# Performance work log

Measured on AMD Instinct MI355X. Metric: run time of the kernel, lower is better.

## Reference

```python
import jax, jax.numpy as jnp
import numpy as np
from jax import lax

MODEL_DIM = 384
KERNEL = 15
PAD = (KERNEL - 1) // 2
BATCH = 4096


def fake_quant(x, bits):
    """Per-tensor symmetric fake quantization with straight-through estimator.
    scale = max|x| / qmax, q = clip(round(x/scale), qmin, qmax), dq = q*scale.
    """
    qmax = float(2 ** (bits - 1) - 1)
    qmin = -float(2 ** (bits - 1))
    scale = jnp.maximum(jnp.max(jnp.abs(x)) / qmax, jnp.asarray(1e-8, x.dtype))
    dq = jnp.clip(jnp.round(x / scale), qmin, qmax) * scale
    return x + lax.stop_gradient(dq - x)  # STE: identity gradient


def setup_inputs() -> dict:
    key = jax.random.key(0)
    k = jax.random.split(key, 7)
    image = jax.random.normal(k[0], (BATCH, 28, 28), dtype=jnp.float32)
    # LinearQuant(28 -> model_dim)
    W1 = jax.random.normal(k[1], (MODEL_DIM, 28), dtype=jnp.float32) * (1.0 / np.sqrt(28))
    b1 = jax.random.normal(k[2], (MODEL_DIM,), dtype=jnp.float32) * 0.01
    # depthwise Conv1DQuant(model_dim, model_dim, K, groups=model_dim): weight [C_out, 1, K]
    Wc = jax.random.normal(k[3], (MODEL_DIM, 1, KERNEL), dtype=jnp.float32) * (1.0 / np.sqrt(KERNEL))
    bc = jax.random.normal(k[4], (MODEL_DIM,), dtype=jnp.float32) * 0.01
    # LinearQuant(28*model_dim -> 10)
    Wf = jax.random.normal(k[5], (10, 28 * MODEL_DIM), dtype=jnp.float32) * (1.0 / np.sqrt(28 * MODEL_DIM))
    bf = jax.random.normal(k[6], (10,), dtype=jnp.float32) * 0.01
    return {"image": image, "W1": W1, "b1": b1, "Wc": Wc, "bc": bc, "Wf": Wf, "bf": bf}


def reference(image, W1, b1, Wc, bc, Wf, bf):
    inp = image.reshape(-1, 28, 28)
    # linear_1 with 8-bit activation fake-quant in and 3-bit weight fake-quant
    x = fake_quant(inp, 8)
    lin = jnp.einsum('blf,of->blo', x, fake_quant(W1, 3)) + b1  # [B,28,model_dim]
    out1 = jnp.tanh(fake_quant(lin, 8))
    # depthwise conv1d over length 28, channels model_dim
    xc = jnp.transpose(fake_quant(out1, 8), (0, 2, 1))  # [B,C,L]
    conv = lax.conv_general_dilated(
        xc, fake_quant(Wc, 3), window_strides=(1,), padding=[(PAD, PAD)],
        dimension_numbers=('NCH', 'OIH', 'NCH'), feature_group_count=MODEL_DIM)
    conv = conv + bc[None, :, None]                      # [B,C,L]
    conv = jnp.transpose(conv, (0, 2, 1))                # [B,L,C]
    out2 = jnp.tanh(fake_quant(conv, 8)).reshape(-1, MODEL_DIM * 28)
    # final linear
    logits = fake_quant(out2, 8) @ fake_quant(Wf, 3).T + bf  # [B,10]
    return fake_quant(logits, 8)
```

## Files before the change

kernel.cpp:

```cpp
#include <hip/hip_runtime.h>

#define BATCH 4096
#define MD 384
#define KW 15
#define PADW 7
#define LSEQ 28
#define FIN 28

#define NX (BATCH*LSEQ*FIN)


#define B_SCF  0
#define B_LUT1 256
#define B_LUT2 512
#define B_PT0  1024
#define B_PT1  33792
#define B_PT2  41984
#define B_PTL  50176
#define B_W1B  54272
#define B_WCQ  78848
#define B_WFB  84992
#define B_LG   192512
#define B_XQB  356352

typedef __bf16 bf16x8 __attribute__((ext_vector_type(8)));
typedef float f32x4 __attribute__((ext_vector_type(4)));
typedef int i32x4 __attribute__((ext_vector_type(4)));

#if __has_builtin(__builtin_amdgcn_sdot4)
#define SDOT4(a,b,c) __builtin_amdgcn_sdot4((a),(b),(c),false)
#else
__device__ __forceinline__ int SDOT4(int a,int b,int c){
  c += ((a<<24)>>24)*((b<<24)>>24);
  c += ((a<<16)>>24)*((b<<16)>>24);
  c += ((a<<8)>>24)*((b<<8)>>24);
  c += (a>>24)*(b>>24);
  return c;
}
#endif

#if __has_builtin(__builtin_amdgcn_alignbyte)
#define ALIGNB(hi,lo,s) __builtin_amdgcn_alignbyte((hi),(lo),(s))
#else
#define ALIGNB(hi,lo,s) ((int)(((unsigned)(lo)>>(8*(s)))|((unsigned)(hi)<<(32-8*(s)))))
#endif

__device__ __forceinline__ unsigned short f2bf(float f){
  return (unsigned short)(__float_as_uint(f)>>16);
}

__device__ __forceinline__ void blkStore4(float m0,float m1,float m2,float m3,float4* dst){
  #pragma unroll
  for(int off=32;off;off>>=1){
    m0=fmaxf(m0,__shfl_xor(m0,off,64));
    m1=fmaxf(m1,__shfl_xor(m1,off,64));
    m2=fmaxf(m2,__shfl_xor(m2,off,64));
    m3=fmaxf(m3,__shfl_xor(m3,off,64));
  }
  __shared__ float sm[4][4];
  int wid=threadIdx.x>>6;
  if((threadIdx.x&63)==0){sm[wid][0]=m0;sm[wid][1]=m1;sm[wid][2]=m2;sm[wid][3]=m3;}
  __syncthreads();
  if(threadIdx.x==0){
    for(int i=1;i<4;i++){
      m0=fmaxf(m0,sm[i][0]);m1=fmaxf(m1,sm[i][1]);
      m2=fmaxf(m2,sm[i][2]);m3=fmaxf(m3,sm[i][3]);
    }
    *dst=make_float4(m0,m1,m2,m3);
  }
}

__device__ __forceinline__ void blkStoreMM(float mn,float mx,float2* dst){
  #pragma unroll
  for(int off=32;off;off>>=1){
    mn=fminf(mn,__shfl_xor(mn,off,64));
    mx=fmaxf(mx,__shfl_xor(mx,off,64));
  }
  __shared__ float smn[8],smx[8];
  int wid=threadIdx.x>>6, nw=blockDim.x>>6;
  if((threadIdx.x&63)==0){smn[wid]=mn;smx[wid]=mx;}
  __syncthreads();
  if(threadIdx.x==0){
    for(int i=1;i<nw;i++){mn=fminf(mn,smn[i]);mx=fmaxf(mx,smx[i]);}
    *dst=make_float2(mn,mx);
  }
}

__global__ __launch_bounds__(256)
void k_maxabs_in(const float* __restrict__ img,const float* __restrict__ W1,
                 const float* __restrict__ Wc,const float* __restrict__ Wf,
                 float4* __restrict__ pt0){
  float m0=0.f,m1=0.f,m2=0.f,m3=0.f;
  const int N4=NX/4;
  const int NW1=MD*FIN, NWC=MD*KW, NWF=10*MD*LSEQ;
  const int total=N4+NW1+NWC+NWF;
  const float4* img4=(const float4*)img;
  for(int i=blockIdx.x*blockDim.x+threadIdx.x;i<total;i+=gridDim.x*blockDim.x){
    if(i<N4){
      float4 v=img4[i];
      m0=fmaxf(m0,fmaxf(fmaxf(fabsf(v.x),fabsf(v.y)),fmaxf(fabsf(v.z),fabsf(v.w))));
    }
    else if(i<N4+NW1) m1=fmaxf(m1,fabsf(W1[i-N4]));
    else if(i<N4+NW1+NWC) m2=fmaxf(m2,fabsf(Wc[i-N4-NW1]));
    else m3=fmaxf(m3,fabsf(Wf[i-N4-NW1-NWC]));
  }
  blkStore4(m0,m1,m2,m3,&pt0[blockIdx.x]);
}

__global__ __launch_bounds__(256)
void k_red0(const float4* __restrict__ pt,float* __restrict__ scf){
  int t=threadIdx.x;
  float m0=0.f,m1=0.f,m2=0.f,m3=0.f;
  for(int i=t;i<2048;i+=256){
    float4 v=pt[i];
    m0=fmaxf(m0,v.x);m1=fmaxf(m1,v.y);m2=fmaxf(m2,v.z);m3=fmaxf(m3,v.w);
  }
  #pragma unroll
  for(int off=32;off;off>>=1){
    m0=fmaxf(m0,__shfl_xor(m0,off,64));
    m1=fmaxf(m1,__shfl_xor(m1,off,64));
    m2=fmaxf(m2,__shfl_xor(m2,off,64));
    m3=fmaxf(m3,__shfl_xor(m3,off,64));
  }
  __shared__ float sm[4][4];
  int wid=t>>6;
  if((t&63)==0){sm[wid][0]=m0;sm[wid][1]=m1;sm[wid][2]=m2;sm[wid][3]=m3;}
  __syncthreads();
  if(t==0){
    for(int i=1;i<4;i++){
      m0=fmaxf(m0,sm[i][0]);m1=fmaxf(m1,sm[i][1]);
      m2=fmaxf(m2,sm[i][2]);m3=fmaxf(m3,sm[i][3]);
    }
    scf[0]=fmaxf(m0/127.f,1e-8f);
    scf[1]=fmaxf(m1/3.f,1e-8f);
    scf[2]=fmaxf(m2/3.f,1e-8f);
    scf[3]=fmaxf(m3/3.f,1e-8f);
  }
}

__global__ __launch_bounds__(256)
void k_redmm(const float2* __restrict__ pt,int n,float* __restrict__ scf,
             int preIdx,int outIdx,char* __restrict__ lutg){
  int t=threadIdx.x;
  float mn=1e30f,mx=-1e30f;
  for(int i=t;i<n;i+=256){
    float2 v=pt[i];
    mn=fminf(mn,v.x); mx=fmaxf(mx,v.y);
  }
  #pragma unroll
  for(int off=32;off;off>>=1){
    mn=fminf(mn,__shfl_xor(mn,off,64));
    mx=fmaxf(mx,__shfl_xor(mx,off,64));
  }
  __shared__ float smn[4],smx[4];
  __shared__ float bs,bso;
  int wid=t>>6;
  if((t&63)==0){smn[wid]=mn;smx[wid]=mx;}
  __syncthreads();
  if(t==0){
    for(int i=1;i<4;i++){mn=fminf(mn,smn[i]);mx=fmaxf(mx,smx[i]);}
    float ma=fmaxf(fabsf(mn),fabsf(mx));
    float s=fmaxf(ma/127.f,1e-8f);
    float a1=fabsf(fminf(fmaxf(rintf(mn/s),-128.f),127.f)*s);
    float a2=fabsf(fminf(fmaxf(rintf(mx/s),-128.f),127.f)*s);
    float so=fmaxf(tanhf(fmaxf(a1,a2))/127.f,1e-8f);
    scf[preIdx]=s; scf[outIdx]=so;
    bs=s; bso=so;
  }
  __syncthreads();
  float d=(float)(t-128)*bs;
  lutg[t]=(char)(int)fminf(fmaxf(rintf(tanhf(d)/bso),-128.f),127.f);
}

__global__ __launch_bounds__(256)
void k_prep(const float* __restrict__ img,const float* __restrict__ W1,
            const float* __restrict__ Wc,const float* __restrict__ Wf,
            const float* __restrict__ scf,char* __restrict__ wsb){
  float s_img=scf[0], s_w1=scf[1], s_wc=scf[2], s_wf=scf[3];
  float inv_img=1.f/s_img;
  unsigned short* xqb=(unsigned short*)(wsb+B_XQB);
  unsigned short* w1b=(unsigned short*)(wsb+B_W1B);
  char* wcpk=wsb+B_WCQ;
  char* wfb=wsb+B_WFB;
  const int T0=BATCH*LSEQ*32;
  const int T1=T0+MD*32;
  const int T2=T1+MD*16;
  const int T3=T2+10*10752;
  for(int i=blockIdx.x*blockDim.x+threadIdx.x;i<T3;i+=gridDim.x*blockDim.x){
    if(i<T0){
      int row=i>>5, cc=i&31;
      float q = cc<FIN ? fminf(fmaxf(rintf(img[row*FIN+cc]*inv_img),-128.f),127.f) : 0.f;
      xqb[i]=f2bf(q);
    } else if(i<T1){
      int j=i-T0; int o=j>>5, cc=j&31;
      float q = cc<FIN ? fminf(fmaxf(rintf(W1[o*FIN+cc]/s_w1),-4.f),3.f) : 0.f;
      w1b[j]=f2bf(q);
    } else if(i<T2){
      int j=i-T1; int c=j>>4, k=j&15;
      char q=0;
      if(k<KW) q=(char)(int)fminf(fmaxf(rintf(Wc[c*KW+k]/s_wc),-4.f),3.f);
      wcpk[j]=q;
    } else {
      int j=i-T2;
      int n=j/10752, r=j-n*10752;
      int c=r/28, l=r-c*28;
      wfb[j]=(char)(int)fminf(fmaxf(rintf(Wf[n*10752+l*MD+c]/s_wf),-4.f),3.f);
    }
  }
}

template<int MODE>
__global__ __launch_bounds__(512)
void k_fused(const unsigned short* __restrict__ xqb,const unsigned short* __restrict__ w1b,
             const float* __restrict__ b1,const float* __restrict__ scf,
             const char* __restrict__ lut1g,const char* __restrict__ lut2g,
             const char* __restrict__ wcpk,const float* __restrict__ bc,
             const int* __restrict__ wfw,const float* __restrict__ bfv,
             float2* __restrict__ ptmm,float* __restrict__ lg,
             float* __restrict__ ptl){
  __shared__ int ldsI[10752];
  __shared__ int psum[10][4][7];
  __shared__ char lutA[256];
  __shared__ char lutB[256];
  int t=threadIdx.x, wid=t>>6, lane=t&63, l4=lane>>4, l15=lane&15;
  {
    const int* src=(const int*)w1b;
    for(int i=t;i<6144;i+=512) ldsI[i]=src[i];
  }
  __syncthreads();
  unsigned short* Wlds=(unsigned short*)ldsI;
  bf16x8 bfr[3]; float b1v[3];
  #pragma unroll
  for(int ni=0;ni<3;ni++){
    int o=(wid*3+ni)*16+l15;
    bfr[ni]=*(const bf16x8*)&Wlds[o*32+l4*8];
    b1v[ni]=b1[o];
  }
  bf16x8 af[7];
  int r0=blockIdx.x*112;
  #pragma unroll
  for(int mt=0;mt<7;mt++)
    af[mt]=*(const bf16x8*)&xqb[(size_t)(r0+mt*16+l15)*32+l4*8];
  float sg=scf[0]*scf[1];
  float inv_lin=1.f, inv_cv=1.f, sfac=1.f, gsc=1.f;
  if constexpr(MODE>=1){
    inv_lin=1.f/scf[4];
    sfac=scf[5]*scf[2];
    if(t<64) ((int*)lutA)[t]=((const int*)lut1g)[t];
  }
  if constexpr(MODE==2){
    inv_cv=1.f/scf[6];
    gsc=scf[3]*scf[7];
    if(t>=64&&t<128) ((int*)lutB)[t-64]=((const int*)lut2g)[t-64];
  }
  if constexpr(MODE>=1) __syncthreads();

  float mn=1e30f,mx=-1e30f;
  f32x4 zero={0.f,0.f,0.f,0.f};
  #pragma unroll
  for(int ni=0;ni<3;ni++){
    int o=(wid*3+ni)*16+l15;
    #pragma unroll
    for(int mt=0;mt<7;mt++){
      f32x4 acc=__builtin_amdgcn_mfma_f32_16x16x32_bf16(af[mt],bfr[ni],zero,0,0,0);
      if constexpr(MODE==0){
        #pragma unroll
        for(int r=0;r<4;r++){
          float v=sg*acc[r]+b1v[ni];
          mn=fminf(mn,v); mx=fmaxf(mx,v);
        }
      } else {
        unsigned w=0;
        #pragma unroll
        for(int r=0;r<4;r++){
          float v=sg*acc[r]+b1v[ni];
          int ql=(int)fminf(fmaxf(rintf(v*inv_lin),-128.f),127.f);
          unsigned q=(unsigned)(unsigned char)lutA[ql+128];
          w|=q<<(8*r);
        }
        ldsI[o*28+mt*4+l4]=(int)w;
      }
    }
  }
  if constexpr(MODE==0){
    blkStoreMM(mn,mx,&ptmm[blockIdx.x]);
    return;
  }
  __syncthreads();

  int oww[3][7];
  float mnc=1e30f,mxc=-1e30f;
  #pragma unroll
  for(int rr=0;rr<3;rr++){
    int j=t+rr*512;
    int s=j/384, c=j-s*384;
    i32x4 wq=*(const i32x4*)(wcpk+(size_t)c*16);
    float bias=bc[c];
    int ext[11];
    ext[0]=0; ext[1]=0; ext[9]=0; ext[10]=0;
    #pragma unroll
    for(int i=0;i<7;i++) ext[2+i]=ldsI[c*28+s*7+i];
    #pragma unroll
    for(int l=0;l<LSEQ;l++){
      const int eb=l+1, bi=eb>>2, sh=eb&3;
      int A0,A1,A2,A3;
      if(sh==0){A0=ext[bi];A1=ext[bi+1];A2=ext[bi+2];A3=ext[bi+3];}
      else{
        A0=ALIGNB(ext[bi+1],ext[bi],sh);
        A1=ALIGNB(ext[bi+2],ext[bi+1],sh);
        A2=ALIGNB(ext[bi+3],ext[bi+2],sh);
        A3=ALIGNB(ext[bi+4],ext[bi+3],sh);
      }
      int idot=SDOT4(A0,wq[0],SDOT4(A1,wq[1],SDOT4(A2,wq[2],SDOT4(A3,wq[3],0))));
      float v=fmaf((float)idot,sfac,bias);
      if constexpr(MODE==1){
        mnc=fminf(mnc,v); mxc=fmaxf(mxc,v);
      } else {
        int qc=(int)fminf(fmaxf(rintf(v*inv_cv),-128.f),127.f);
        unsigned q2=(unsigned)(unsigned char)lutB[qc+128];
        if((l&3)==0) oww[rr][l>>2]=(int)q2;
        else oww[rr][l>>2]|=(int)(q2<<(8*(l&3)));
      }
    }
  }
  if constexpr(MODE==1){
    blkStoreMM(mnc,mxc,&ptmm[blockIdx.x]);
    return;
  }

  __syncthreads();
  #pragma unroll
  for(int rr=0;rr<3;rr++){
    int j=t+rr*512;
    int s=j/384, c=j-s*384;
    #pragma unroll
    for(int i=0;i<7;i++) ldsI[s*2688+c*7+i]=oww[rr][i];
  }
  __syncthreads();

  if(t<448){
    int cwv[24];
    #pragma unroll
    for(int s=0;s<4;s++)
      #pragma unroll
      for(int j6=0;j6<6;j6++) cwv[s*6+j6]=ldsI[s*2688+j6*448+t];
    #pragma unroll
    for(int o=0;o<10;o++){
      int a0=0,a1=0,a2=0,a3=0;
      #pragma unroll
      for(int j6=0;j6<6;j6++){
        int wfv=wfw[o*2688+j6*448+t];
        a0=SDOT4(cwv[0*6+j6],wfv,a0);
        a1=SDOT4(cwv[1*6+j6],wfv,a1);
        a2=SDOT4(cwv[2*6+j6],wfv,a2);
        a3=SDOT4(cwv[3*6+j6],wfv,a3);
      }
      #pragma unroll
      for(int off=32;off;off>>=1){
        a0+=__shfl_xor(a0,off,64);
        a1+=__shfl_xor(a1,off,64);
        a2+=__shfl_xor(a2,off,64);
        a3+=__shfl_xor(a3,off,64);
      }
      if(lane==0){
        psum[o][0][wid]=a0; psum[o][1][wid]=a1;
        psum[o][2][wid]=a2; psum[o][3][wid]=a3;
      }
    }
  }
  __syncthreads();
  float m=0.f;
  if(t<40){
    int s=t/10, o=t-s*10;
    int sum=0;
    #pragma unroll
    for(int i=0;i<7;i++) sum+=psum[o][s][i];
    float v=fmaf((float)sum,gsc,bfv[o]);
    lg[(blockIdx.x*4+s)*10+o]=v;
    m=fabsf(v);
  }
  if(t<64){
    #pragma unroll
    for(int off=32;off;off>>=1) m=fmaxf(m,__shfl_xor(m,off,64));
    if(t==0) ptl[blockIdx.x]=m;
  }
}

__global__ __launch_bounds__(256)
void k_final(const float* __restrict__ lg,const float* __restrict__ ptl,
             float* __restrict__ out){
  int t=threadIdx.x;
  float m=0.f;
  for(int i=t;i<1024;i+=256) m=fmaxf(m,ptl[i]);
  #pragma unroll
  for(int off=32;off;off>>=1) m=fmaxf(m,__shfl_xor(m,off,64));
  __shared__ float sm[4];
  __shared__ float sv;
  int wid=t>>6;
  if((t&63)==0) sm[wid]=m;
  __syncthreads();
  if(t==0){
    for(int k=1;k<4;k++) m=fmaxf(m,sm[k]);
    sv=fmaxf(m/127.f,1e-8f);
  }
  __syncthreads();
  float s=sv;
  int i=blockIdx.x*256+t;
  out[i]=fminf(fmaxf(rintf(lg[i]/s),-128.f),127.f)*s;
}

extern "C" void kernel_launch(void* const* d_in, const int* in_sizes, int n_in,
                              void* d_out, int out_size, void* d_ws, size_t ws_size,
                              hipStream_t stream){
  const float* img=(const float*)d_in[0];
  const float* W1 =(const float*)d_in[1];
  const float* b1 =(const float*)d_in[2];
  const float* Wc =(const float*)d_in[3];
  const float* bc =(const float*)d_in[4];
  const float* Wf =(const float*)d_in[5];
  const float* bf =(const float*)d_in[6];
  float* out=(float*)d_out;
  char* wsb=(char*)d_ws;
  float* scf=(float*)(wsb+B_SCF);
  float4* pt0=(float4*)(wsb+B_PT0);
  float2* pt1=(float2*)(wsb+B_PT1);
  float2* pt2=(float2*)(wsb+B_PT2);
  float* ptl=(float*)(wsb+B_PTL);
  float* lg=(float*)(wsb+B_LG);
  const unsigned short* xqb=(const unsigned short*)(wsb+B_XQB);
  const unsigned short* w1b=(const unsigned short*)(wsb+B_W1B);
  const char* wcpk=wsb+B_WCQ;
  const int* wfw=(const int*)(wsb+B_WFB);

  k_maxabs_in<<<2048,256,0,stream>>>(img,W1,Wc,Wf,pt0);
  k_red0<<<1,256,0,stream>>>(pt0,scf);
  k_prep<<<4096,256,0,stream>>>(img,W1,Wc,Wf,scf,wsb);
  k_fused<0><<<1024,512,0,stream>>>(xqb,w1b,b1,scf,nullptr,nullptr,wcpk,bc,wfw,bf,pt1,nullptr,nullptr);
  k_redmm<<<1,256,0,stream>>>(pt1,1024,scf,4,5,wsb+B_LUT1);
  k_fused<1><<<1024,512,0,stream>>>(xqb,w1b,b1,scf,wsb+B_LUT1,nullptr,wcpk,bc,wfw,bf,pt2,nullptr,nullptr);
  k_redmm<<<1,256,0,stream>>>(pt2,1024,scf,6,7,wsb+B_LUT2);
  k_fused<2><<<1024,512,0,stream>>>(xqb,w1b,b1,scf,wsb+B_LUT1,wsb+B_LUT2,wcpk,bc,wfw,bf,nullptr,lg,ptl);
  k_final<<<160,256,0,stream>>>(lg,ptl,out);
}
```

Before: 107.7 us.

## Use int8 MFMA for final linear, bpermute LUTs, hoisted min/max and padded LDS

The final 10-output linear layer now runs on int8 MFMA (16x16x64) over a byte-laid-out weight buffer instead of per-thread sdot4 with wave shuffle reductions. The LDS lookup tables are replaced by per-wave ds_bpermute lookups from a register-held 256-byte table. Scale and bias are folded into a single fma with a med3 clamp. The min/max passes now track raw accumulator extremes and apply the affine transform once at the end. LDS row strides are padded (29, 2692) to reduce bank conflicts, and the workspace offsets are moved to hold the larger weight buffer. This depends on k_prep writing Wf in the layout the new MFMA reads, which is not visible here.

Result: faster. 105.6 us (-2.0%).

```diff
diff --git a/kernel.cpp b/kernel.cpp
--- a/kernel.cpp
+++ b/kernel.cpp
@@ -20,8 +20,8 @@
 #define B_W1B  54272
 #define B_WCQ  78848
 #define B_WFB  84992
-#define B_LG   192512
-#define B_XQB  356352
+#define B_LG   257024
+#define B_XQB  420864
 
 typedef __bf16 bf16x8 __attribute__((ext_vector_type(8)));
 typedef float f32x4 __attribute__((ext_vector_type(4)));
@@ -47,6 +47,11 @@
 
 __device__ __forceinline__ unsigned short f2bf(float f){
   return (unsigned short)(__float_as_uint(f)>>16);
+}
+
+__device__ __forceinline__ unsigned lut_bperm(int iw,int lutw){
+  int res=__builtin_amdgcn_ds_bpermute(iw,lutw);
+  return ((unsigned)res>>(8*(iw&3)))&0xFFu;
 }
 
 __device__ __forceinline__ void blkStore4(float m0,float m1,float m2,float m3,float4* dst){
@@ -209,19 +214,19 @@
   }
 }
 
+#define CWS 29
+#define DWS 2692
 template<int MODE>
 __global__ __launch_bounds__(512)
 void k_fused(const unsigned short* __restrict__ xqb,const unsigned short* __restrict__ w1b,
              const float* __restrict__ b1,const float* __restrict__ scf,
              const char* __restrict__ lut1g,const char* __restrict__ lut2g,
              const char* __restrict__ wcpk,const float* __restrict__ bc,
-             const int* __restrict__ wfw,const float* __restrict__ bfv,
+             const char* __restrict__ wfb,const float* __restrict__ bfv,
              float2* __restrict__ ptmm,float* __restrict__ lg,
              float* __restrict__ ptl){
-  __shared__ int ldsI[10752];
-  __shared__ int psum[10][4][7];
-  __shared__ char lutA[256];
-  __shared__ char lutB[256];
+  __shared__ int ldsI[MD*CWS];
+  __shared__ int psumN[8][10][4];
   int t=threadIdx.x, wid=t>>6, lane=t&63, l4=lane>>4, l15=lane&15;
   {
     const int* src=(const int*)w1b;
@@ -242,21 +247,28 @@
   for(int mt=0;mt<7;mt++)
     af[mt]=*(const bf16x8*)&xqb[(size_t)(r0+mt*16+l15)*32+l4*8];
   float sg=scf[0]*scf[1];
-  float inv_lin=1.f, inv_cv=1.f, sfac=1.f, gsc=1.f;
+  float sgi=sg, b1s[3]={0.f,0.f,0.f};
+  int lutA_w=0,lutB_w=0;
+  float ck1=1.f,inv_cv=1.f,sfac=1.f,gsc=1.f;
   if constexpr(MODE>=1){
-    inv_lin=1.f/scf[4];
+    float inv_lin=1.f/scf[4];
+    sgi=sg*inv_lin;
+    #pragma unroll
+    for(int ni=0;ni<3;ni++) b1s[ni]=fmaf(b1v[ni],inv_lin,128.f);
+    lutA_w=((const int*)lut1g)[lane];
     sfac=scf[5]*scf[2];
-    if(t<64) ((int*)lutA)[t]=((const int*)lut1g)[t];
   }
   if constexpr(MODE==2){
     inv_cv=1.f/scf[6];
+    ck1=sfac*inv_cv;
     gsc=scf[3]*scf[7];
-    if(t>=64&&t<128) ((int*)lutB)[t-64]=((const int*)lut2g)[t-64];
+    lutB_w=((const int*)lut2g)[lane];
   }
   if constexpr(MODE>=1) __syncthreads();
 
+  f32x4 zero={0.f,0.f,0.f,0.f};
   float mn=1e30f,mx=-1e30f;
-  f32x4 zero={0.f,0.f,0.f,0.f};
+  float mnn[3]={1e30f,1e30f,1e30f},mxx[3]={-1e30f,-1e30f,-1e30f};
   #pragma unroll
   for(int ni=0;ni<3;ni++){
     int o=(wid*3+ni)*16+l15;
@@ -266,23 +278,26 @@
       if constexpr(MODE==0){
         #pragma unroll
         for(int r=0;r<4;r++){
-          float v=sg*acc[r]+b1v[ni];
-          mn=fminf(mn,v); mx=fmaxf(mx,v);
+          mnn[ni]=fminf(mnn[ni],acc[r]); mxx[ni]=fmaxf(mxx[ni],acc[r]);
         }
       } else {
         unsigned w=0;
         #pragma unroll
         for(int r=0;r<4;r++){
-          float v=sg*acc[r]+b1v[ni];
-          int ql=(int)fminf(fmaxf(rintf(v*inv_lin),-128.f),127.f);
-          unsigned q=(unsigned)(unsigned char)lutA[ql+128];
-          w|=q<<(8*r);
+          float x=fmaf(acc[r],sgi,b1s[ni]);
+          int iw=(int)__builtin_amdgcn_fmed3f(rintf(x),0.f,255.f);
+          w|=lut_bperm(iw,lutA_w)<<(8*r);
         }
-        ldsI[o*28+mt*4+l4]=(int)w;
+        ldsI[o*CWS+mt*4+l4]=(int)w;
       }
     }
   }
   if constexpr(MODE==0){
+    #pragma unroll
+    for(int ni=0;ni<3;ni++){
+      mn=fminf(mn,fmaf(mnn[ni],sg,b1v[ni]));
+      mx=fmaxf(mx,fmaf(mxx[ni],sg,b1v[ni]));
+    }
     blkStoreMM(mn,mx,&ptmm[blockIdx.x]);
     return;
   }
@@ -295,11 +310,14 @@
     int j=t+rr*512;
     int s=j/384, c=j-s*384;
     i32x4 wq=*(const i32x4*)(wcpk+(size_t)c*16);
-    float bias=bc[c];
+    float cbias=bc[c];
+    float cq2=0.f;
+    if constexpr(MODE==2) cq2=fmaf(cbias,inv_cv,128.f);
     int ext[11];
     ext[0]=0; ext[1]=0; ext[9]=0; ext[10]=0;
     #pragma unroll
-    for(int i=0;i<7;i++) ext[2+i]=ldsI[c*28+s*7+i];
+    for(int i=0;i<7;i++) ext[2+i]=ldsI[c*CWS+s*7+i];
+    int imn=0x7FFFFFFF,imx=0x80000000;
     #pragma unroll
     for(int l=0;l<LSEQ;l++){
       const int eb=l+1, bi=eb>>2, sh=eb&3;
@@ -312,16 +330,20 @@
         A3=ALIGNB(ext[bi+4],ext[bi+3],sh);
       }
       int idot=SDOT4(A0,wq[0],SDOT4(A1,wq[1],SDOT4(A2,wq[2],SDOT4(A3,wq[3],0))));
-      float v=fmaf((float)idot,sfac,bias);
       if constexpr(MODE==1){
-        mnc=fminf(mnc,v); mxc=fmaxf(mxc,v);
+        imn=min(imn,idot); imx=max(imx,idot);
       } else {
-        int qc=(int)fminf(fmaxf(rintf(v*inv_cv),-128.f),127.f);
-        unsigned q2=(unsigned)(unsigned char)lutB[qc+128];
+        float x=fmaf((float)idot,ck1,cq2);
+        int iw=(int)__builtin_amdgcn_fmed3f(rintf(x),0.f,255.f);
+        unsigned q2=lut_bperm(iw,lutB_w);
         if((l&3)==0) oww[rr][l>>2]=(int)q2;
         else oww[rr][l>>2]|=(int)(q2<<(8*(l&3)));
       }
     }
+    if constexpr(MODE==1){
+      mnc=fminf(mnc,fmaf((float)imn,sfac,cbias));
+      mxc=fmaxf(mxc,fmaf((float)imx,sfac,cbias));
+    }
   }
   if constexpr(MODE==1){
     blkStoreMM(mnc,mxc,&ptmm[blockIdx.x]);
@@ -334,38 +356,21 @@
     int j=t+rr*512;
     int s=j/384, c=j-s*384;
     #pragma unroll
-    for(int i=0;i<7;i++) ldsI[s*2688+c*7+i]=oww[rr][i];
-  }
-  __syncthreads();
-
-  if(t<448){
-    int cwv[24];
-    #pragma unroll
-    for(int s=0;s<4;s++)
+    for(int i=0;i<7;i++) ldsI[s*DWS+c*7+i]=oww[rr][i];
+  }
+  __syncthreads();
+
+  {
+    i32x4 acc={0,0,0,0};
+    const char* ldsB=(const char*)ldsI;
+    for(int kb=wid;kb<168;kb+=8){
+      i32x4 a=*(const i32x4*)(ldsB+(size_t)(l15&3)*(DWS*4)+kb*64+l4*16);
+      i32x4 b=*(const i32x4*)(wfb+(size_t)l15*10752+kb*64+l4*16);
+      acc=__builtin_amdgcn_mfma_i32_16x16x64_i8(a,b,acc,0,0,0);
+    }
+    if(l4==0&&l15<10){
       #pragma unroll
-      for(int j6=0;j6<6;j6++) cwv[s*6+j6]=ldsI[s*2688+j6*448+t];
-    #pragma unroll
-    for(int o=0;o<10;o++){
-      int a0=0,a1=0,a2=0,a3=0;
-      #pragma unroll
-      for(int j6=0;j6<6;j6++){
-        int wfv=wfw[o*2688+j6*448+t];
-        a0=SDOT4(cwv[0*6+j6],wfv,a0);
-        a1=SDOT4(cwv[1*6+j6],wfv,a1);
-        a2=SDOT4(cwv[2*6+j6],wfv,a2);
-        a3=SDOT4(cwv[3*6+j6],wfv,a3);
-      }
-      #pragma unroll
-      for(int off=32;off;off>>=1){
-        a0+=__shfl_xor(a0,off,64);
-        a1+=__shfl_xor(a1,off,64);
-        a2+=__shfl_xor(a2,off,64);
-        a3+=__shfl_xor(a3,off,64);
-      }
-      if(lane==0){
-        psum[o][0][wid]=a0; psum[o][1][wid]=a1;
-        psum[o][2][wid]=a2; psum[o][3][wid]=a3;
-      }
+      for(int r=0;r<4;r++) psumN[wid][l15][r]=acc[r];
     }
   }
   __syncthreads();
@@ -374,7 +379,7 @@
     int s=t/10, o=t-s*10;
     int sum=0;
     #pragma unroll
-    for(int i=0;i<7;i++) sum+=psum[o][s][i];
+    for(int w=0;w<8;w++) sum+=psumN[w][o][s];
     float v=fmaf((float)sum,gsc,bfv[o]);
     lg[(blockIdx.x*4+s)*10+o]=v;
     m=fabsf(v);
@@ -430,15 +435,15 @@
   const unsigned short* xqb=(const unsigned short*)(wsb+B_XQB);
   const unsigned short* w1b=(const unsigned short*)(wsb+B_W1B);
   const char* wcpk=wsb+B_WCQ;
-  const int* wfw=(const int*)(wsb+B_WFB);
+  const char* wfb=wsb+B_WFB;
 
   k_maxabs_in<<<2048,256,0,stream>>>(img,W1,Wc,Wf,pt0);
   k_red0<<<1,256,0,stream>>>(pt0,scf);
   k_prep<<<4096,256,0,stream>>>(img,W1,Wc,Wf,scf,wsb);
-  k_fused<0><<<1024,512,0,stream>>>(xqb,w1b,b1,scf,nullptr,nullptr,wcpk,bc,wfw,bf,pt1,nullptr,nullptr);
+  k_fused<0><<<1024,512,0,stream>>>(xqb,w1b,b1,scf,nullptr,nullptr,wcpk,bc,wfb,bf,pt1,nullptr,nullptr);
   k_redmm<<<1,256,0,stream>>>(pt1,1024,scf,4,5,wsb+B_LUT1);
-  k_fused<1><<<1024,512,0,stream>>>(xqb,w1b,b1,scf,wsb+B_LUT1,nullptr,wcpk,bc,wfw,bf,pt2,nullptr,nullptr);
+  k_fused<1><<<1024,512,0,stream>>>(xqb,w1b,b1,scf,wsb+B_LUT1,nullptr,wcpk,bc,wfb,bf,pt2,nullptr,nullptr);
   k_redmm<<<1,256,0,stream>>>(pt2,1024,scf,6,7,wsb+B_LUT2);
-  k_fused<2><<<1024,512,0,stream>>>(xqb,w1b,b1,scf,wsb+B_LUT1,wsb+B_LUT2,wcpk,bc,wfw,bf,nullptr,lg,ptl);
+  k_fused<2><<<1024,512,0,stream>>>(xqb,w1b,b1,scf,wsb+B_LUT1,wsb+B_LUT2,wcpk,bc,wfb,bf,nullptr,lg,ptl);
   k_final<<<160,256,0,stream>>>(lg,ptl,out);
 }
```
